# Performance work log

Measured on AMD Instinct MI355X. Metric: run time of the kernel, lower is better.

Reference implementation:

```python
import jax, jax.numpy as jnp
import numpy as np

B, T = 4, 2048          # batch, seq_len
D, H = 2048, 4096       # input_dim, router hidden_dim
E, O = 16, 2048         # num_experts, expert_output_dim
TAU = 0.5               # forward default tau


def setup_inputs() -> dict:
    key = jax.random.key(0)
    kx, k1, k2, k3, k4, k5, k6 = jax.random.split(key, 7)
    s = 0.02
    return {
        "x": jax.random.normal(kx, (B, T, D), dtype=jnp.float32),
        "W1": jax.random.normal(k1, (D, H), dtype=jnp.float32) * s,
        "b1": jnp.zeros((H,), dtype=jnp.float32),
        "W2": jax.random.normal(k2, (H, E), dtype=jnp.float32) * s,
        "b2": jnp.zeros((E,), dtype=jnp.float32),
        "We": jax.random.normal(k3, (E, D, O), dtype=jnp.float32) * s,
        "be": jnp.zeros((E, O), dtype=jnp.float32),
    }


def reference(x, W1, b1, W2, b2, We, be):
    # Router: Linear -> ReLU -> Linear -> softmax
    h = jax.nn.relu(jnp.einsum("btd,dh->bth", x, W1) + b1)
    logits = jnp.einsum("bth,he->bte", h, W2) + b2
    probs = jax.nn.softmax(logits, axis=-1)                 # [B,T,E]
    max_p = jnp.max(probs, axis=-1, keepdims=True)
    mask = probs >= TAU * max_p                              # [B,T,E] bool
    k_per_token = jnp.sum(mask, axis=-1)                     # [B,T] int
    gates = jnp.where(mask, probs, 0.0)                      # masked router probs
    # Per-expert dense Linear, masked weighted accumulate (E=16 is a fixed,
    # structurally distinct set; loop is over experts, not data dims).
    out = jnp.zeros((B, T, O), dtype=x.dtype)
    for i in range(E):
        expert_out = jnp.einsum("btd,do->bto", x, We[i]) + be[i]
        out = out + gates[..., i:i + 1] * expert_out
    return out, k_per_token
```

## Files before the change

kernel.cpp:

```cpp
#include <hip/hip_runtime.h>
#include <stdint.h>

#define M_TOK 8192
#define DDIM  2048
#define HDIM  4096
#define NEXP  16
#define ODIM  2048

typedef __attribute__((ext_vector_type(8))) __bf16 bf16x8;
typedef __attribute__((ext_vector_type(4))) float  f32x4;

__device__ __forceinline__ unsigned short f2bf(float f) {
    unsigned int u = __float_as_uint(f);
    unsigned int r = (u + 0x7FFFu + ((u >> 16) & 1u)) >> 16;
    return (unsigned short)r;
}
__device__ __forceinline__ float bf2f(unsigned short s) {
    return __uint_as_float(((unsigned int)s) << 16);
}

template <int CTRL>
__device__ __forceinline__ float dpp_mov(float x) {
    return __int_as_float(
        __builtin_amdgcn_update_dpp(0, __float_as_int(x), CTRL, 0xF, 0xF, true));
}
__device__ __forceinline__ float swz_xor4(float x) {
    return __int_as_float(__builtin_amdgcn_ds_swizzle(__float_as_int(x), 0x101F));
}


__global__ void split_x_kernel(const float* __restrict__ x,
                               ushort* __restrict__ xh, ushort* __restrict__ xl) {
    size_t i = ((size_t)blockIdx.x * 256 + threadIdx.x) * 4;
    float4 v = *(const float4*)(x + i);
    float f[4] = {v.x, v.y, v.z, v.w};
    ushort hu[4], lu[4];
#pragma unroll
    for (int u = 0; u < 4; ++u) {
        hu[u] = f2bf(f[u]);
        lu[u] = f2bf(f[u] - bf2f(hu[u]));
    }
    *(ushort4*)(xh + i) = make_ushort4(hu[0], hu[1], hu[2], hu[3]);
    *(ushort4*)(xl + i) = make_ushort4(lu[0], lu[1], lu[2], lu[3]);
}

__global__ void transpose_split_w1_kernel(const float* __restrict__ W1,
                                          ushort* __restrict__ th, ushort* __restrict__ tl) {
    __shared__ float tile[64][65];
    int h0 = (blockIdx.x & 63) * 64;
    int d0 = (blockIdx.x >> 6) * 64;
    int r = threadIdx.x >> 4;
    int c = (threadIdx.x & 15) * 4;
#pragma unroll
    for (int rr = 0; rr < 4; ++rr) {
        int row = rr * 16 + r;
        float4 v = *(const float4*)(W1 + (size_t)(d0 + row) * HDIM + h0 + c);
        tile[row][c + 0] = v.x; tile[row][c + 1] = v.y;
        tile[row][c + 2] = v.z; tile[row][c + 3] = v.w;
    }
    __syncthreads();
#pragma unroll
    for (int rr = 0; rr < 4; ++rr) {
        int hrow = rr * 16 + r;
        ushort hu[4], lu[4];
#pragma unroll
        for (int u = 0; u < 4; ++u) {
            float f = tile[c + u][hrow];
            hu[u] = f2bf(f);
            lu[u] = f2bf(f - bf2f(hu[u]));
        }
        size_t o = (size_t)(h0 + hrow) * DDIM + d0 + c;
        *(ushort4*)(th + o) = make_ushort4(hu[0], hu[1], hu[2], hu[3]);
        *(ushort4*)(tl + o) = make_ushort4(lu[0], lu[1], lu[2], lu[3]);
    }
}

__global__ void transpose_we_kernel(const float* __restrict__ We, ushort* __restrict__ wt) {
    __shared__ float tile[64][65];
    int e = blockIdx.y;
    int o0 = (blockIdx.x & 31) * 64;
    int d0 = (blockIdx.x >> 5) * 64;
    const float* src = We + (size_t)e * DDIM * ODIM;
    ushort* dst = wt + (size_t)e * ODIM * DDIM;
    int r = threadIdx.x >> 4;
    int c = (threadIdx.x & 15) * 4;
#pragma unroll
    for (int rr = 0; rr < 4; ++rr) {
        int row = rr * 16 + r;
        float4 v = *(const float4*)(src + (size_t)(d0 + row) * ODIM + o0 + c);
        tile[row][c + 0] = v.x; tile[row][c + 1] = v.y;
        tile[row][c + 2] = v.z; tile[row][c + 3] = v.w;
    }
    __syncthreads();
#pragma unroll
    for (int rr = 0; rr < 4; ++rr) {
        int orow = rr * 16 + r;
        ushort hu[4];
#pragma unroll
        for (int u = 0; u < 4; ++u) hu[u] = f2bf(tile[c + u][orow]);
        *(ushort4*)(dst + (size_t)(o0 + orow) * DDIM + d0 + c) =
            make_ushort4(hu[0], hu[1], hu[2], hu[3]);
    }
}


__device__ __forceinline__ void stage_tile(const ushort* __restrict__ g0, int ld,
                                           ushort* lds0, int wave, int lane) {
#pragma unroll
    for (int j = 0; j < 4; ++j) {
        int L = wave * 256 + j * 64 + lane;
        int m = L >> 3;
        int kc = (L & 7) ^ (m & 7);
        const ushort* gp = g0 + (size_t)m * ld + kc * 8;
        ushort* lp = lds0 + (size_t)(wave * 256 + j * 64) * 8;
        __builtin_amdgcn_global_load_lds(
            (const __attribute__((address_space(1))) void*)gp,
            (__attribute__((address_space(3))) void*)lp, 16, 0, 0);
    }
}

__device__ __forceinline__ bf16x8 ldfrag(const ushort* lds0, int row, int kc) {
    return *(const bf16x8*)(lds0 + ((row << 3) + (kc ^ (row & 7))) * 8);
}

__device__ __forceinline__ void mfma_step(const ushort* As, const ushort* Bs,
                                          int wm, int wn, int mrow, int q,
                                          f32x4 (&acc)[4][4]) {
#pragma unroll
    for (int s = 0; s < 2; ++s) {
        bf16x8 af[4], bfr[4];
#pragma unroll
        for (int i = 0; i < 4; ++i) af[i] = ldfrag(As, wm + i * 16 + mrow, s * 4 + q);
#pragma unroll
        for (int j = 0; j < 4; ++j) bfr[j] = ldfrag(Bs, wn + j * 16 + mrow, s * 4 + q);
#pragma unroll
        for (int i = 0; i < 4; ++i)
#pragma unroll
            for (int j = 0; j < 4; ++j)
                acc[i][j] = __builtin_amdgcn_mfma_f32_16x16x32_bf16(
                    af[i], bfr[j], acc[i][j], 0, 0, 0);
    }
}

__global__ __launch_bounds__(512, 2) void gemm1_kernel(
    const ushort* __restrict__ xh, const ushort* __restrict__ xl,
    const ushort* __restrict__ wh, const ushort* __restrict__ wl,
    const float* __restrict__ b1, const float* __restrict__ W2,
    float* __restrict__ logits) {
    __shared__ ushort lds[65536];
    ushort* const A0 = lds;
    ushort* const B0 = lds + 16384;
    ushort* const A1 = lds + 32768;
    ushort* const B1 = lds + 49152;

    const int tile_m = (blockIdx.x >> 4) << 8;
    const int tile_n = (blockIdx.x & 15) << 8;
    const int tid = threadIdx.x;
    const int wave = tid >> 6, lane = tid & 63;
    const int q = lane >> 4, mrow = lane & 15;
    const int wr = (wave >> 2) << 7;
    const int wcb = (wave & 3) << 6;

    unsigned goff[4];
    int ldso[4];
#pragma unroll
    for (int j = 0; j < 4; ++j) {
        int L = wave * 256 + j * 64 + lane;
        int m = L >> 3;
        int kc = (L & 7) ^ (m & 7);
        goff[j] = (unsigned)m * DDIM + kc * 8;
        ldso[j] = L * 8;
    }

    f32x4 acc[8][4];
#pragma unroll
    for (int i = 0; i < 8; ++i)
#pragma unroll
        for (int j = 0; j < 4; ++j) acc[i][j] = {0.f, 0.f, 0.f, 0.f};

#define SRC_A(t) ((((t) >> 5) == 1 ? xl : xh) + (size_t)tile_m * DDIM + (((t) & 31) << 6))
#define SRC_B(t) ((((t) >> 5) == 2 ? wl : wh) + (size_t)tile_n * DDIM + (((t) & 31) << 6))
#define STAGE(srcp, dstp)                                                           \
    {                                                                               \
        const ushort* _s = (srcp);                                                  \
        ushort* _d = (dstp);                                                        \
        _Pragma("unroll")                                                           \
        for (int _j = 0; _j < 4; ++_j)                                              \
            __builtin_amdgcn_global_load_lds(                                       \
                (const __attribute__((address_space(1))) void*)(_s + goff[_j]),     \
                (__attribute__((address_space(3))) void*)(_d + ldso[_j]), 16, 0, 0);\
    }

    STAGE(SRC_A(0), A0); STAGE(SRC_B(0), B0);
    STAGE(SRC_A(1), A1); STAGE(SRC_B(1), B1);
    asm volatile("s_waitcnt vmcnt(8)" ::: "memory");
    __builtin_amdgcn_s_barrier();
    __builtin_amdgcn_sched_barrier(0);

    for (int kt = 0; kt < 96; ++kt) {
        ushort* As = (kt & 1) ? A1 : A0;
        ushort* Bs = (kt & 1) ? B1 : B0;
        bf16x8 a0[8], a1[8], bv0[4], bv1[4];
#pragma unroll
        for (int i = 0; i < 8; ++i) {
            a0[i] = ldfrag(As, wr + i * 16 + mrow, q);
            a1[i] = ldfrag(As, wr + i * 16 + mrow, 4 + q);
        }
#pragma unroll
        for (int j = 0; j < 4; ++j) {
            bv0[j] = ldfrag(Bs, wcb + j * 16 + mrow, q);
            bv1[j] = ldfrag(Bs, wcb + j * 16 + mrow, 4 + q);
        }
        asm volatile("s_waitcnt lgkmcnt(0)" ::: "memory");
        __builtin_amdgcn_sched_barrier(0);
        __builtin_amdgcn_s_barrier();
        __builtin_amdgcn_sched_barrier(0);
        if (kt + 2 < 96) {
            STAGE(SRC_A(kt + 2), As);
            STAGE(SRC_B(kt + 2), Bs);
        }
#pragma unroll
        for (int i = 0; i < 8; ++i)
#pragma unroll
            for (int j = 0; j < 4; ++j)
                acc[i][j] = __builtin_amdgcn_mfma_f32_16x16x32_bf16(
                    a0[i], bv0[j], acc[i][j], 0, 0, 0);
#pragma unroll
        for (int i = 0; i < 8; ++i)
#pragma unroll
            for (int j = 0; j < 4; ++j)
                acc[i][j] = __builtin_amdgcn_mfma_f32_16x16x32_bf16(
                    a1[i], bv1[j], acc[i][j], 0, 0, 0);
        if (kt + 2 < 96) {
            asm volatile("s_waitcnt vmcnt(8)" ::: "memory");
        } else {
            asm volatile("s_waitcnt vmcnt(0)" ::: "memory");
        }
        __builtin_amdgcn_s_barrier();
        __builtin_amdgcn_sched_barrier(0);
    }
#undef SRC_A
#undef SRC_B
#undef STAGE

    float b1v[4];
    f32x4 w2r[4][4];
#pragma unroll
    for (int j = 0; j < 4; ++j) {
        const int cc = tile_n + wcb + j * 16 + mrow;
        b1v[j] = b1[cc];
        const float4* wp = (const float4*)(W2 + (size_t)cc * NEXP);
#pragma unroll
        for (int qq = 0; qq < 4; ++qq) {
            float4 v = wp[qq];
            w2r[j][qq] = (f32x4){v.x, v.y, v.z, v.w};
        }
    }
    __syncthreads();
    float* part = (float*)lds;
    const int pw = wave & 3;
    const bool pb0 = (mrow & 1) != 0, pb1 = (mrow & 2) != 0;
    const bool pb2 = (mrow & 4) != 0, pb3 = (mrow & 8) != 0;
    const int E = (mrow & 3) | ((mrow & 8) >> 1) | ((mrow & 4) << 1);
#pragma unroll
    for (int i = 0; i < 8; ++i) {
#pragma unroll
        for (int r = 0; r < 4; ++r) {
            const int rl = wr + i * 16 + q * 4 + r;
            float ll[16];
#pragma unroll
            for (int e = 0; e < 16; ++e) ll[e] = 0.f;
#pragma unroll
            for (int j = 0; j < 4; ++j) {
                float v = acc[i][j][r] + b1v[j];
                v = v > 0.f ? v : 0.f;
#pragma unroll
                for (int e = 0; e < 16; ++e)
                    ll[e] = fmaf(v, w2r[j][e >> 2][e & 3], ll[e]);
            }
            float s1[8];
#pragma unroll
            for (int e2 = 0; e2 < 8; ++e2) {
                float a = ll[2 * e2], b = ll[2 * e2 + 1];
                float y = pb0 ? b : a, z = pb0 ? a : b;
                s1[e2] = y + dpp_mov<0xB1>(z);
            }
            float s2[4];
#pragma unroll
            for (int e2 = 0; e2 < 4; ++e2) {
                float a = s1[2 * e2], b = s1[2 * e2 + 1];
                float y = pb1 ? b : a, z = pb1 ? a : b;
                s2[e2] = y + dpp_mov<0x4E>(z);
            }
            float s3[2];
#pragma unroll
            for (int e2 = 0; e2 < 2; ++e2) {
                float a = s2[2 * e2], b = s2[2 * e2 + 1];
                float y = pb3 ? b : a, z = pb3 ? a : b;
                s3[e2] = y + dpp_mov<0x128>(z);
            }
            {
                float a = s3[0], b = s3[1];
                float y = pb2 ? b : a, z = pb2 ? a : b;
                float fin = y + swz_xor4(z);
                part[((size_t)(pw << 8) + rl) * 16 + E] = fin;
            }
        }
    }
    __syncthreads();
    for (int idx = tid; idx < 4096; idx += 512) {
        float s = part[idx] + part[4096 + idx] + part[8192 + idx] + part[12288 + idx];
        atomicAdd(&logits[(size_t)(tile_m + (idx >> 4)) * NEXP + (idx & 15)], s);
    }
}

__global__ void gates_kernel(const float* __restrict__ logits,
                             const float* __restrict__ b2,
                             float* __restrict__ gates, float* __restrict__ kout,
                             int* __restrict__ cnt, int* __restrict__ list) {
    const int t = blockIdx.x * 256 + threadIdx.x;
    float l[16];
    const float4* lp = (const float4*)(logits + (size_t)t * 16);
#pragma unroll
    for (int i = 0; i < 4; ++i) {
        float4 v = lp[i];
        l[i * 4] = v.x; l[i * 4 + 1] = v.y; l[i * 4 + 2] = v.z; l[i * 4 + 3] = v.w;
    }
#pragma unroll
    for (int i = 0; i < 16; ++i) l[i] += b2[i];
    float lmax = l[0];
#pragma unroll
    for (int i = 1; i < 16; ++i) lmax = fmaxf(lmax, l[i]);
    float p[16], S = 0.f;
#pragma unroll
    for (int i = 0; i < 16; ++i) { p[i] = expf(l[i] - lmax); S += p[i]; }
#pragma unroll
    for (int i = 0; i < 16; ++i) p[i] /= S;
    float pmax = p[0];
#pragma unroll
    for (int i = 1; i < 16; ++i) pmax = fmaxf(pmax, p[i]);
    const float thr = 0.5f * pmax;
    int k = 0;
    float g[16];
#pragma unroll
    for (int i = 0; i < 16; ++i) {
        bool m = p[i] >= thr;
        g[i] = m ? p[i] : 0.f;
        k += m ? 1 : 0;
        if (m) {
            int pos = atomicAdd(&cnt[i], 1);
            list[i * M_TOK + pos] = t;
        }
    }
    float4* gp = (float4*)(gates + (size_t)t * 16);
#pragma unroll
    for (int i = 0; i < 4; ++i)
        gp[i] = make_float4(g[i * 4], g[i * 4 + 1], g[i * 4 + 2], g[i * 4 + 3]);
    kout[t] = (float)k;
}

__global__ void init_out_kernel(const float* __restrict__ gates,
                                const float* __restrict__ be, float* __restrict__ out) {
    const int t = blockIdx.x;
    const int tid = threadIdx.x;
    __shared__ float g[16];
    if (tid < 16) g[tid] = gates[(size_t)t * 16 + tid];
    __syncthreads();
    const int c0 = tid * 8;
    float a[8] = {0.f, 0.f, 0.f, 0.f, 0.f, 0.f, 0.f, 0.f};
#pragma unroll
    for (int e = 0; e < 16; ++e) {
        float ge = g[e];
        if (ge != 0.f) {
            float4 v1 = *(const float4*)(be + (size_t)e * ODIM + c0);
            float4 v2 = *(const float4*)(be + (size_t)e * ODIM + c0 + 4);
            a[0] = fmaf(ge, v1.x, a[0]); a[1] = fmaf(ge, v1.y, a[1]);
            a[2] = fmaf(ge, v1.z, a[2]); a[3] = fmaf(ge, v1.w, a[3]);
            a[4] = fmaf(ge, v2.x, a[4]); a[5] = fmaf(ge, v2.y, a[5]);
            a[6] = fmaf(ge, v2.z, a[6]); a[7] = fmaf(ge, v2.w, a[7]);
        }
    }
    *(float4*)(out + (size_t)t * ODIM + c0)     = make_float4(a[0], a[1], a[2], a[3]);
    *(float4*)(out + (size_t)t * ODIM + c0 + 4) = make_float4(a[4], a[5], a[6], a[7]);
}

__global__ __launch_bounds__(256, 3) void moe_sparse_kernel(
    const ushort* __restrict__ xh, const ushort* __restrict__ weT,
    const float* __restrict__ gates, const int* __restrict__ cnt,
    const int* __restrict__ list, float* __restrict__ out) {
    const int bx = blockIdx.x;
    const int e = bx >> 10;
    const int chunk = (bx >> 4) & 63;
    const int ntile = bx & 15;
    const int ce = cnt[e];
    const int row0 = chunk << 7;
    if (row0 >= ce) return;
    const int rows = min(128, ce - row0);

    __shared__ ushort As[8192];
    __shared__ ushort Bs[8192];
    __shared__ int toks[128];
    __shared__ float gv[128];

    const int tid = threadIdx.x;
    if (tid < 128) {
        int t = list[e * M_TOK + row0 + min(tid, rows - 1)];
        toks[tid] = t;
        gv[tid] = gates[(size_t)t * NEXP + e];
    }
    __syncthreads();

    const int wave = tid >> 6, lane = tid & 63;
    const int q = lane >> 4, mrow = lane & 15;
    const int wm = (wave >> 1) << 6, wn = (wave & 1) << 6;

    const ushort* agp[4];
    const ushort* bgp[4];
    ushort* alp[4];
    ushort* blp[4];
    const ushort* wbase = weT + ((size_t)e * ODIM + (ntile << 7)) * DDIM;
#pragma unroll
    for (int j = 0; j < 4; ++j) {
        int L = wave * 256 + j * 64 + lane;
        int m = L >> 3;
        int kc = (L & 7) ^ (m & 7);
        agp[j] = xh + (size_t)toks[m] * DDIM + kc * 8;
        bgp[j] = wbase + (size_t)m * DDIM + kc * 8;
        alp[j] = As + (size_t)L * 8;
        blp[j] = Bs + (size_t)L * 8;
    }

    f32x4 acc[4][4];
#pragma unroll
    for (int i = 0; i < 4; ++i)
#pragma unroll
        for (int j = 0; j < 4; ++j) acc[i][j] = {0.f, 0.f, 0.f, 0.f};

    for (int it = 0; it < 32; ++it) {
        const int k0 = it << 6;
        __syncthreads();
#pragma unroll
        for (int j = 0; j < 4; ++j) {
            __builtin_amdgcn_global_load_lds(
                (const __attribute__((address_space(1))) void*)(agp[j] + k0),
                (__attribute__((address_space(3))) void*)alp[j], 16, 0, 0);
            __builtin_amdgcn_global_load_lds(
                (const __attribute__((address_space(1))) void*)(bgp[j] + k0),
                (__attribute__((address_space(3))) void*)blp[j], 16, 0, 0);
        }
        __syncthreads();
        mfma_step(As, Bs, wm, wn, mrow, q, acc);
    }

#pragma unroll
    for (int i = 0; i < 4; ++i) {
        const int rl = wm + i * 16 + q * 4;
#pragma unroll
        for (int r = 0; r < 4; ++r) {
            const int lrow = rl + r;
            if (lrow < rows) {
                const int t = toks[lrow];
                const float g = gv[lrow];
                float* orow = out + (size_t)t * ODIM + (ntile << 7) + wn + mrow;
#pragma unroll
                for (int j = 0; j < 4; ++j)
                    atomicAdd(orow + j * 16, g * acc[i][j][r]);
            }
        }
    }
}

extern "C" void kernel_launch(void* const* d_in, const int* in_sizes, int n_in,
                              void* d_out, int out_size, void* d_ws, size_t ws_size,
                              hipStream_t stream) {
    const float* x  = (const float*)d_in[0];
    const float* W1 = (const float*)d_in[1];
    const float* b1 = (const float*)d_in[2];
    const float* W2 = (const float*)d_in[3];
    const float* b2 = (const float*)d_in[4];
    const float* We = (const float*)d_in[5];
    const float* be = (const float*)d_in[6];
    float* out  = (float*)d_out;
    float* kout = out + (size_t)M_TOK * ODIM;

    char* ws = (char*)d_ws;
    ushort* x_hi   = (ushort*)(ws);
    ushort* x_lo   = (ushort*)(ws + 33554432);
    ushort* w1t_hi = (ushort*)(ws + 67108864);
    ushort* w1t_lo = (ushort*)(ws + 83886080);
    int*    cnt    = (int*)   (ws + 83886080);
    int*    list   = (int*)   (ws + 83887104);
    ushort* weT    = (ushort*)(ws + 100663296);
    float*  logits = (float*) (ws + 234881024);
    float*  gates  = (float*) (ws + 235405312);

    hipMemsetAsync(logits, 0, (size_t)M_TOK * NEXP * sizeof(float), stream);
    split_x_kernel<<<16384, 256, 0, stream>>>(x, x_hi, x_lo);
    transpose_split_w1_kernel<<<2048, 256, 0, stream>>>(W1, w1t_hi, w1t_lo);
    gemm1_kernel<<<512, 512, 0, stream>>>(x_hi, x_lo, w1t_hi, w1t_lo, b1, W2, logits);
    hipMemsetAsync(cnt, 0, 64, stream);
    gates_kernel<<<32, 256, 0, stream>>>(logits, b2, gates, kout, cnt, list);
    dim3 gwe(1024, 16);
    transpose_we_kernel<<<gwe, 256, 0, stream>>>(We, weT);
    init_out_kernel<<<M_TOK, 256, 0, stream>>>(gates, be, out);
    moe_sparse_kernel<<<16384, 256, 0, stream>>>(x_hi, weT, gates, cnt, list, out);
}
```

Measured before the change: 1.198 ms.

## Enlarge MoE expert GEMM tiles to 256x256 with double-buffered async LDS staging

The sparse expert GEMM moves from 128x128 tiles with 256 threads and a single LDS buffer to 256x256 tiles with 512 threads. Tiles are staged through double-buffered global_load_lds with explicit vmcnt waits, the same pipeline the router GEMM already uses. This aims to raise data reuse per tile and overlap global loads with MFMA work. In exchange, per-expert row padding waste grows with the larger tile, fewer blocks launch, and register and LDS pressure per block goes up.

```diff
diff --git a/kernel.cpp b/kernel.cpp
--- a/kernel.cpp
+++ b/kernel.cpp
@@ -104,42 +104,8 @@
 }
 
 
-__device__ __forceinline__ void stage_tile(const ushort* __restrict__ g0, int ld,
-                                           ushort* lds0, int wave, int lane) {
-#pragma unroll
-    for (int j = 0; j < 4; ++j) {
-        int L = wave * 256 + j * 64 + lane;
-        int m = L >> 3;
-        int kc = (L & 7) ^ (m & 7);
-        const ushort* gp = g0 + (size_t)m * ld + kc * 8;
-        ushort* lp = lds0 + (size_t)(wave * 256 + j * 64) * 8;
-        __builtin_amdgcn_global_load_lds(
-            (const __attribute__((address_space(1))) void*)gp,
-            (__attribute__((address_space(3))) void*)lp, 16, 0, 0);
-    }
-}
-
 __device__ __forceinline__ bf16x8 ldfrag(const ushort* lds0, int row, int kc) {
     return *(const bf16x8*)(lds0 + ((row << 3) + (kc ^ (row & 7))) * 8);
-}
-
-__device__ __forceinline__ void mfma_step(const ushort* As, const ushort* Bs,
-                                          int wm, int wn, int mrow, int q,
-                                          f32x4 (&acc)[4][4]) {
-#pragma unroll
-    for (int s = 0; s < 2; ++s) {
-        bf16x8 af[4], bfr[4];
-#pragma unroll
-        for (int i = 0; i < 4; ++i) af[i] = ldfrag(As, wm + i * 16 + mrow, s * 4 + q);
-#pragma unroll
-        for (int j = 0; j < 4; ++j) bfr[j] = ldfrag(Bs, wn + j * 16 + mrow, s * 4 + q);
-#pragma unroll
-        for (int i = 0; i < 4; ++i)
-#pragma unroll
-            for (int j = 0; j < 4; ++j)
-                acc[i][j] = __builtin_amdgcn_mfma_f32_16x16x32_bf16(
-                    af[i], bfr[j], acc[i][j], 0, 0, 0);
-    }
 }
 
 __global__ __launch_bounds__(512, 2) void gemm1_kernel(
@@ -241,7 +207,6 @@
     }
 #undef SRC_A
 #undef SRC_B
-#undef STAGE
 
     float b1v[4];
     f32x4 w2r[4][4];
@@ -384,26 +349,29 @@
     *(float4*)(out + (size_t)t * ODIM + c0 + 4) = make_float4(a[4], a[5], a[6], a[7]);
 }
 
-__global__ __launch_bounds__(256, 3) void moe_sparse_kernel(
+__global__ __launch_bounds__(512, 2) void moe_sparse_kernel(
     const ushort* __restrict__ xh, const ushort* __restrict__ weT,
     const float* __restrict__ gates, const int* __restrict__ cnt,
     const int* __restrict__ list, float* __restrict__ out) {
     const int bx = blockIdx.x;
-    const int e = bx >> 10;
-    const int chunk = (bx >> 4) & 63;
-    const int ntile = bx & 15;
+    const int e = bx >> 8;
+    const int chunk = (bx >> 3) & 31;
+    const int ntile = bx & 7;
     const int ce = cnt[e];
-    const int row0 = chunk << 7;
+    const int row0 = chunk << 8;
     if (row0 >= ce) return;
-    const int rows = min(128, ce - row0);
-
-    __shared__ ushort As[8192];
-    __shared__ ushort Bs[8192];
-    __shared__ int toks[128];
-    __shared__ float gv[128];
+    const int rows = min(256, ce - row0);
+
+    __shared__ ushort lds[65536];
+    __shared__ int toks[256];
+    __shared__ float gv[256];
+    ushort* const A0 = lds;
+    ushort* const B0 = lds + 16384;
+    ushort* const A1 = lds + 32768;
+    ushort* const B1 = lds + 49152;
 
     const int tid = threadIdx.x;
-    if (tid < 128) {
+    if (tid < 256) {
         int t = list[e * M_TOK + row0 + min(tid, rows - 1)];
         toks[tid] = t;
         gv[tid] = gates[(size_t)t * NEXP + e];
@@ -412,13 +380,13 @@
 
     const int wave = tid >> 6, lane = tid & 63;
     const int q = lane >> 4, mrow = lane & 15;
-    const int wm = (wave >> 1) << 6, wn = (wave & 1) << 6;
+    const int wr = (wave >> 2) << 7;
+    const int wcb = (wave & 3) << 6;
 
     const ushort* agp[4];
     const ushort* bgp[4];
-    ushort* alp[4];
-    ushort* blp[4];
-    const ushort* wbase = weT + ((size_t)e * ODIM + (ntile << 7)) * DDIM;
+    int ldso[4];
+    const ushort* wbase = weT + ((size_t)e * ODIM + (ntile << 8)) * DDIM;
 #pragma unroll
     for (int j = 0; j < 4; ++j) {
         int L = wave * 256 + j * 64 + lane;
@@ -426,42 +394,85 @@
         int kc = (L & 7) ^ (m & 7);
         agp[j] = xh + (size_t)toks[m] * DDIM + kc * 8;
         bgp[j] = wbase + (size_t)m * DDIM + kc * 8;
-        alp[j] = As + (size_t)L * 8;
-        blp[j] = Bs + (size_t)L * 8;
-    }
-
-    f32x4 acc[4][4];
-#pragma unroll
-    for (int i = 0; i < 4; ++i)
+        ldso[j] = L * 8;
+    }
+
+    f32x4 acc[8][4];
+#pragma unroll
+    for (int i = 0; i < 8; ++i)
 #pragma unroll
         for (int j = 0; j < 4; ++j) acc[i][j] = {0.f, 0.f, 0.f, 0.f};
 
-    for (int it = 0; it < 32; ++it) {
-        const int k0 = it << 6;
-        __syncthreads();
+#define MSTAGE(gp, dstp, k0)                                                        \
+    {                                                                               \
+        ushort* _d = (dstp);                                                        \
+        _Pragma("unroll")                                                           \
+        for (int _j = 0; _j < 4; ++_j)                                              \
+            __builtin_amdgcn_global_load_lds(                                       \
+                (const __attribute__((address_space(1))) void*)(gp[_j] + (k0)),     \
+                (__attribute__((address_space(3))) void*)(_d + ldso[_j]), 16, 0, 0);\
+    }
+
+    MSTAGE(agp, A0, 0); MSTAGE(bgp, B0, 0);
+    MSTAGE(agp, A1, 64); MSTAGE(bgp, B1, 64);
+    asm volatile("s_waitcnt vmcnt(8)" ::: "memory");
+    __builtin_amdgcn_s_barrier();
+    __builtin_amdgcn_sched_barrier(0);
+
+    for (int kt = 0; kt < 32; ++kt) {
+        ushort* As = (kt & 1) ? A1 : A0;
+        ushort* Bs = (kt & 1) ? B1 : B0;
+        bf16x8 a0[8], a1[8], bv0[4], bv1[4];
+#pragma unroll
+        for (int i = 0; i < 8; ++i) {
+            a0[i] = ldfrag(As, wr + i * 16 + mrow, q);
+            a1[i] = ldfrag(As, wr + i * 16 + mrow, 4 + q);
+        }
 #pragma unroll
         for (int j = 0; j < 4; ++j) {
-            __builtin_amdgcn_global_load_lds(
-                (const __attribute__((address_space(1))) void*)(agp[j] + k0),
-                (__attribute__((address_space(3))) void*)alp[j], 16, 0, 0);
-            __builtin_amdgcn_global_load_lds(
-                (const __attribute__((address_space(1))) void*)(bgp[j] + k0),
-                (__attribute__((address_space(3))) void*)blp[j], 16, 0, 0);
-        }
-        __syncthreads();
-        mfma_step(As, Bs, wm, wn, mrow, q, acc);
-    }
-
-#pragma unroll
-    for (int i = 0; i < 4; ++i) {
-        const int rl = wm + i * 16 + q * 4;
+            bv0[j] = ldfrag(Bs, wcb + j * 16 + mrow, q);
+            bv1[j] = ldfrag(Bs, wcb + j * 16 + mrow, 4 + q);
+        }
+        asm volatile("s_waitcnt lgkmcnt(0)" ::: "memory");
+        __builtin_amdgcn_sched_barrier(0);
+        __builtin_amdgcn_s_barrier();
+        __builtin_amdgcn_sched_barrier(0);
+        if (kt + 2 < 32) {
+            MSTAGE(agp, As, (kt + 2) * 64);
+            MSTAGE(bgp, Bs, (kt + 2) * 64);
+        }
+#pragma unroll
+        for (int i = 0; i < 8; ++i)
+#pragma unroll
+            for (int j = 0; j < 4; ++j)
+                acc[i][j] = __builtin_amdgcn_mfma_f32_16x16x32_bf16(
+                    a0[i], bv0[j], acc[i][j], 0, 0, 0);
+#pragma unroll
+        for (int i = 0; i < 8; ++i)
+#pragma unroll
+            for (int j = 0; j < 4; ++j)
+                acc[i][j] = __builtin_amdgcn_mfma_f32_16x16x32_bf16(
+                    a1[i], bv1[j], acc[i][j], 0, 0, 0);
+        if (kt + 2 < 32) {
+            asm volatile("s_waitcnt vmcnt(8)" ::: "memory");
+        } else {
+            asm volatile("s_waitcnt vmcnt(0)" ::: "memory");
+        }
+        __builtin_amdgcn_s_barrier();
+        __builtin_amdgcn_sched_barrier(0);
+    }
+#undef MSTAGE
+
+#pragma unroll
+    for (int i = 0; i < 8; ++i) {
+        const int rl = wr + i * 16 + q * 4;
 #pragma unroll
         for (int r = 0; r < 4; ++r) {
             const int lrow = rl + r;
             if (lrow < rows) {
                 const int t = toks[lrow];
                 const float g = gv[lrow];
-                float* orow = out + (size_t)t * ODIM + (ntile << 7) + wn + mrow;
+                float* orow = out + (size_t)t * ODIM + (ntile << 8) + wcb + mrow;
 #pragma unroll
                 for (int j = 0; j < 4; ++j)
                     atomicAdd(orow + j * 16, g * acc[i][j][r]);
@@ -503,5 +514,5 @@
     dim3 gwe(1024, 16);
     transpose_we_kernel<<<gwe, 256, 0, stream>>>(We, weT);
     init_out_kernel<<<M_TOK, 256, 0, stream>>>(gates, be, out);
-    moe_sparse_kernel<<<16384, 256, 0, stream>>>(x_hi, weT, gates, cnt, list, out);
-}
+    moe_sparse_kernel<<<4096, 512, 0, stream>>>(x_hi, weT, gates, cnt, list, out);
+}
```

Measured after the change: 1.267 ms. 5.8% more time.
